# Optimization experiments

Hardware: AMD Instinct MI355X
Metric: run time of the kernel (lower is better)

## Reference

```python
import jax, jax.numpy as jnp
import numpy as np

NEG_INF = -1e12  # matches masked_fill value -1000000000000.0
LEAKY_SLOPE = 0.2


def setup_inputs() -> dict:
    key = jax.random.key(0)
    k1, k2, k3, k4, k5 = jax.random.split(key, 5)
    B, C, H, N, F_IN, F_OUT = 4, 4, 4, 1024, 64, 64
    h = jax.random.normal(k1, (B, C, N, F_IN), dtype=jnp.float32)
    adj = jax.random.randint(k2, (B, N, N), 0, 2).astype(jnp.float32)
    w = jax.random.normal(k3, (C, H, F_IN, F_OUT), dtype=jnp.float32) * 0.1
    a_src = jax.random.normal(k4, (C, H, F_OUT, 1), dtype=jnp.float32) * 0.1
    a_dst = jax.random.normal(k5, (C, H, F_OUT, 1), dtype=jnp.float32) * 0.1
    return {"h": h, "adj": adj, "w": w, "a_src": a_src, "a_dst": a_dst}


def reference(h, adj, w, a_src, a_dst):
    # h: [B,C,N,f_in], w: [C,H,f_in,f_out] -> h_prime: [B,C,H,N,f_out]
    h_prime = jnp.einsum('bcnf,chfo->bchno', h, w)
    t = jnp.tanh(h_prime)
    # additive attention scores: [B,C,H,N]
    attn_src = jnp.einsum('bchno,cho->bchn', t, a_src[..., 0])
    attn_dst = jnp.einsum('bchno,cho->bchn', t, a_dst[..., 0])
    # attn[b,c,h,i,j] = src[i] + dst[j]  -> [B,C,H,N,N]
    attn = attn_src[..., :, None] + attn_dst[..., None, :]
    attn = jnp.where(attn >= 0, attn, LEAKY_SLOPE * attn)  # leaky_relu(0.2)
    N = h.shape[2]
    adj_sl = adj + jnp.eye(N, dtype=adj.dtype)  # add self-loops
    mask = (adj_sl == 0)[:, None, None, :, :]   # [B,1,1,N,N]
    attn = jnp.where(mask, NEG_INF, attn)
    attn = jax.nn.softmax(attn, axis=-1)
    # dropout is identity (attn_dropout=0.0 / eval mode)
    out = jnp.einsum('bchnm,bchmo->bchno', attn, h_prime)
    return out
```

## Files before the change

### kernel.cpp

```cpp
#include <hip/hip_runtime.h>
#include <hip/hip_bf16.h>
#include <math.h>

#define NB 4
#define NC 4
#define NH 4
#define NN 1024
#define NF 64
#define NCOMBO 64
#define LEAK 0.2f

typedef __attribute__((ext_vector_type(8)))  short  short8;
typedef __attribute__((ext_vector_type(16))) float  float16;

static __device__ __forceinline__ unsigned pk_bf16(float a, float b) {
    union { __hip_bfloat162 h; unsigned u; } cv;
    cv.h = __float22bfloat162_rn(make_float2(a, b));
    return cv.u;
}

static __device__ __forceinline__ float fast_tanh(float x) {
    const float e = __expf(2.f * x);
    return 1.f - 2.f * __builtin_amdgcn_rcpf(1.f + e);
}

static __device__ __forceinline__ void async_cp16(const void* gsrc, void* ldst) {
    __builtin_amdgcn_global_load_lds(
        (const __attribute__((address_space(1))) unsigned int*)gsrc,
        (__attribute__((address_space(3))) unsigned int*)ldst, 16, 0, 0);
}

__global__ __launch_bounds__(256) void gA_produce(
    const float* __restrict__ h, const float* __restrict__ adj,
    const float* __restrict__ w, const float* __restrict__ a_src,
    const float* __restrict__ a_dst,
    unsigned short* __restrict__ hpt, float* __restrict__ asrc,
    float* __restrict__ edPt, float* __restrict__ edNt,
    unsigned long long* __restrict__ bits)
{
    __shared__ __align__(16) char smem[33536];
    float* hT     = (float*)smem;
    float* w_s    = (float*)(smem + 16640);
    float* as_lds = (float*)(smem + 33024);
    float* ad_lds = (float*)(smem + 33280);

    const int idx  = blockIdx.x;
    const int t    = threadIdx.x;
    const int g    = (idx & 7)*8 + ((idx >> 3) & 7);
    const int tile = idx >> 6;
    const int b = g >> 4, c = (g >> 2) & 3, hh = g & 3;
    const int tr = t >> 4, tc = t & 15;

    const float4* wsrc = (const float4*)(w + ((size_t)(c*NH + hh))*NF*NF);
    #pragma unroll
    for (int i = 0; i < 4; ++i)
        ((float4*)w_s)[t + i*256] = wsrc[t + i*256];
    if (t < NF) {
        as_lds[t] = a_src[(c*NH + hh)*NF + t];
        ad_lds[t] = a_dst[(c*NH + hh)*NF + t];
    }
    const float* hsrc = h + (((size_t)(b*NC + c))*NN + tile*64)*NF;
    #pragma unroll
    for (int i = 0; i < 4; ++i) {
        const int r = (t >> 4) + i*16, f4 = (t & 15)*4;
        const float4 v = *(const float4*)&hsrc[r*NF + f4];
        hT[(f4+0)*65 + r] = v.x; hT[(f4+1)*65 + r] = v.y;
        hT[(f4+2)*65 + r] = v.z; hT[(f4+3)*65 + r] = v.w;
    }
    __syncthreads();

    float acc[4][4] = {{0.f}};
    #pragma unroll 8
    for (int f = 0; f < 64; ++f) {
        const float4 hv = *(const float4*)&hT[f*65 + tr*4];
        const float4 wv = *(const float4*)&w_s[f*64 + tc*4];
        acc[0][0] = fmaf(hv.x, wv.x, acc[0][0]);
        acc[0][1] = fmaf(hv.x, wv.y, acc[0][1]);
        acc[0][2] = fmaf(hv.x, wv.z, acc[0][2]);
        acc[0][3] = fmaf(hv.x, wv.w, acc[0][3]);
        acc[1][0] = fmaf(hv.y, wv.x, acc[1][0]);
        acc[1][1] = fmaf(hv.y, wv.y, acc[1][1]);
        acc[1][2] = fmaf(hv.y, wv.z, acc[1][2]);
        acc[1][3] = fmaf(hv.y, wv.w, acc[1][3]);
        acc[2][0] = fmaf(hv.z, wv.x, acc[2][0]);
        acc[2][1] = fmaf(hv.z, wv.y, acc[2][1]);
        acc[2][2] = fmaf(hv.z, wv.z, acc[2][2]);
        acc[2][3] = fmaf(hv.z, wv.w, acc[2][3]);
        acc[3][0] = fmaf(hv.w, wv.x, acc[3][0]);
        acc[3][1] = fmaf(hv.w, wv.y, acc[3][1]);
        acc[3][2] = fmaf(hv.w, wv.z, acc[3][2]);
        acc[3][3] = fmaf(hv.w, wv.w, acc[3][3]);
    }

    float ps[4] = {0.f,0.f,0.f,0.f}, pd[4] = {0.f,0.f,0.f,0.f};
    #pragma unroll
    for (int r = 0; r < 4; ++r)
        #pragma unroll
        for (int cc = 0; cc < 4; ++cc) {
            const float tt = fast_tanh(acc[r][cc]);
            ps[r] = fmaf(tt, as_lds[tc*4+cc], ps[r]);
            pd[r] = fmaf(tt, ad_lds[tc*4+cc], pd[r]);
        }
    __syncthreads();
    float* redS = (float*)smem;
    float* redD = redS + 1024;
    #pragma unroll
    for (int r = 0; r < 4; ++r) {
        redS[(tr*4+r)*16 + tc] = ps[r];
        redD[(tr*4+r)*16 + tc] = pd[r];
    }
    __syncthreads();
    if (t < 64) {
        float4 s0 = *(const float4*)&redS[t*16],   s1 = *(const float4*)&redS[t*16+4];
        float4 s2 = *(const float4*)&redS[t*16+8], s3 = *(const float4*)&redS[t*16+12];
        asrc[(size_t)g*NN + tile*64 + t] =
            (s0.x+s0.y+s0.z+s0.w) + (s1.x+s1.y+s1.z+s1.w) +
            (s2.x+s2.y+s2.z+s2.w) + (s3.x+s3.y+s3.z+s3.w);
        float4 d0 = *(const float4*)&redD[t*16],   d1 = *(const float4*)&redD[t*16+4];
        float4 d2 = *(const float4*)&redD[t*16+8], d3 = *(const float4*)&redD[t*16+12];
        const float dsum =
            (d0.x+d0.y+d0.z+d0.w) + (d1.x+d1.y+d1.z+d1.w) +
            (d2.x+d2.y+d2.z+d2.w) + (d3.x+d3.y+d3.z+d3.w);
        edPt[(size_t)g*NN + tile*64 + t] = __expf(dsum);
        edNt[(size_t)g*NN + tile*64 + t] = __expf(LEAK*dsum);
    }
    #pragma unroll
    for (int cc = 0; cc < 4; ++cc) {
        const int o = tc*4 + cc;
        const int pos = (((((tr>>2)*2 + (o>>5))*2 + ((tr>>1)&1))*32 + (o&31))*8)
                        + (tr&1)*4;
        uint2 pk;
        pk.x = pk_bf16(acc[0][cc], acc[1][cc]);
        pk.y = pk_bf16(acc[2][cc], acc[3][cc]);
        *(uint2*)&hpt[((size_t)g*16 + tile)*4096 + pos] = pk;
    }

    {
        const int base = idx*4096;
        #pragma unroll
        for (int q = 0; q < 16; ++q) {
            const int e  = base + q*256 + t;
            const int j  = e & (NN-1);
            const int i  = (e >> 10) & (NN-1);
            const int bb = e >> 20;
            const bool pred = (adj[e] != 0.f) || (j == i);
            const unsigned long long m = __ballot(pred);
            if ((t & 63) == 0) bits[((size_t)bb*NN + i)*16 + (j >> 6)] = m;
        }
    }
}

__global__ __launch_bounds__(256, 4) void gC_attn(
    const unsigned short* __restrict__ hpt, const float* __restrict__ asrc,
    const float* __restrict__ edPt, const float* __restrict__ edNt,
    const unsigned long long* __restrict__ bits, float* __restrict__ out)
{
    __shared__ __align__(16) char smem[29696];
    unsigned short* fragB = (unsigned short*)smem;
    unsigned*       tbl   = (unsigned*)(smem + 16384);
    float*          comb  = (float*)smem;
    unsigned long long* bits_lds = (unsigned long long*)(smem + 20480);
    float*          psum2 = (float*)(smem + 29184);

    const int idx = blockIdx.x;
    const int t   = threadIdx.x;
    const int g   = (idx & 7)*8 + ((idx >> 3) & 7);
    const int it  = idx >> 6;
    const int b   = g >> 4;
    const int i0  = it*64;
    const int wv = t >> 6, lane = t & 63;
    const int l31 = lane & 31, half = lane >> 5;
    const int rg = wv >> 1, jh = wv & 1;
    const int myrow = rg*32 + l31;

    {
        const char* gs = (const char*)hpt + ((size_t)g*16)*8192 + wv*2048 + lane*16;
        char* ls = smem + wv*2048;
        async_cp16(gs, ls);
        async_cp16(gs + 1024, ls + 1024);
    }
    #pragma unroll
    for (int q = 0; q < 4; ++q) {
        const int j = q*256 + t;
        tbl[j] = pk_bf16(edNt[(size_t)g*NN + j], edPt[(size_t)g*NN + j]);
    }
    {
        const unsigned long long* bsrc = bits + ((size_t)b*NN + i0)*16;
        #pragma unroll
        for (int q = 0; q < 4; ++q) {
            const int e = q*256 + t;
            bits_lds[(e >> 4)*17 + (e & 15)] = bsrc[e];
        }
    }
    const float sv    = asrc[(size_t)g*NN + i0 + myrow];
    const float ratio = __expf((LEAK - 1.f)*sv);

    union { short8 v; unsigned short u[8]; } ONES;
    #pragma unroll
    for (int i = 0; i < 8; ++i) ONES.u[i] = 0x3F80;

    float16 acc0, acc1, acc2;
    #pragma unroll
    for (int i = 0; i < 16; ++i) { acc0[i] = 0.f; acc1[i] = 0.f; acc2[i] = 0.f; }

    for (int jt = 0; jt < 16; ++jt) {
        __syncthreads();
        const int fb = jt & 1;
        if (jt < 15) {
            const char* gs = (const char*)hpt + ((size_t)g*16 + jt + 1)*8192
                             + wv*2048 + lane*16;
            char* ls = smem + ((jt + 1) & 1)*8192 + wv*2048;
            async_cp16(gs, ls);
            async_cp16(gs + 1024, ls + 1024);
        }
        const unsigned long long wb = bits_lds[myrow*17 + jt];

        #pragma unroll
        for (int kk = 0; kk < 2; ++kk) {
            const int ks = jh*2 + kk;
            const int jo = ks*16 + half*8;
            const uint4 Ta = *(const uint4*)&tbl[jt*64 + jo];
            const uint4 Tb = *(const uint4*)&tbl[jt*64 + jo + 4];
            const short8 b0 = *(const short8*)
                &fragB[fb*4096 + (((ks*2 + 0)*2 + half)*32 + l31)*8];
            const short8 b1 = *(const short8*)
                &fragB[fb*4096 + (((ks*2 + 1)*2 + half)*32 + l31)*8];
            const unsigned bb = (unsigned)(wb >> jo) & 0xffu;

            float p0, p1, p2, p3, p4, p5, p6, p7;
            {
                union { unsigned u; float f; } hi, lo;
                hi.u = Ta.x & 0xffff0000u; lo.u = Ta.x << 16;
                p0 = fmaxf(hi.f, ratio*lo.f); p0 = (bb & 1u)   ? p0 : 0.f;
                hi.u = Ta.y & 0xffff0000u; lo.u = Ta.y << 16;
                p1 = fmaxf(hi.f, ratio*lo.f); p1 = (bb & 2u)   ? p1 : 0.f;
                hi.u = Ta.z & 0xffff0000u; lo.u = Ta.z << 16;
                p2 = fmaxf(hi.f, ratio*lo.f); p2 = (bb & 4u)   ? p2 : 0.f;
                hi.u = Ta.w & 0xffff0000u; lo.u = Ta.w << 16;
                p3 = fmaxf(hi.f, ratio*lo.f); p3 = (bb & 8u)   ? p3 : 0.f;
                hi.u = Tb.x & 0xffff0000u; lo.u = Tb.x << 16;
                p4 = fmaxf(hi.f, ratio*lo.f); p4 = (bb & 16u)  ? p4 : 0.f;
                hi.u = Tb.y & 0xffff0000u; lo.u = Tb.y << 16;
                p5 = fmaxf(hi.f, ratio*lo.f); p5 = (bb & 32u)  ? p5 : 0.f;
                hi.u = Tb.z & 0xffff0000u; lo.u = Tb.z << 16;
                p6 = fmaxf(hi.f, ratio*lo.f); p6 = (bb & 64u)  ? p6 : 0.f;
                hi.u = Tb.w & 0xffff0000u; lo.u = Tb.w << 16;
                p7 = fmaxf(hi.f, ratio*lo.f); p7 = (bb & 128u) ? p7 : 0.f;
            }

            union { short8 v; unsigned u[4]; } af;
            af.u[0] = pk_bf16(p0, p1);
            af.u[1] = pk_bf16(p2, p3);
            af.u[2] = pk_bf16(p4, p5);
            af.u[3] = pk_bf16(p6, p7);

            acc2 = __builtin_amdgcn_mfma_f32_32x32x16_bf16(af.v, ONES.v, acc2, 0, 0, 0);
            acc0 = __builtin_amdgcn_mfma_f32_32x32x16_bf16(af.v, b0,     acc0, 0, 0, 0);
            acc1 = __builtin_amdgcn_mfma_f32_32x32x16_bf16(af.v, b1,     acc1, 0, 0, 0);
        }
    }

    __syncthreads();

    if (l31 == 0) {
        #pragma unroll
        for (int reg = 0; reg < 16; ++reg) {
            const int r = (reg & 3) + 8*(reg >> 2) + 4*half;
            psum2[jh*64 + rg*32 + r] = acc2[reg];
        }
    }
    if (jh == 1) {
        float* cb = comb + (rg*64 + lane)*34;
        #pragma unroll
        for (int i = 0; i < 8; ++i) {
            float2 v0; v0.x = acc0[2*i]; v0.y = acc0[2*i+1];
            float2 v1; v1.x = acc1[2*i]; v1.y = acc1[2*i+1];
            *(float2*)&cb[2*i]      = v0;
            *(float2*)&cb[16 + 2*i] = v1;
        }
    }
    __syncthreads();
    if (jh == 0) {
        const float* cb = comb + (rg*64 + lane)*34;
        #pragma unroll
        for (int i = 0; i < 8; ++i) {
            const float2 v0 = *(const float2*)&cb[2*i];
            const float2 v1 = *(const float2*)&cb[16 + 2*i];
            acc0[2*i] += v0.x; acc0[2*i+1] += v0.y;
            acc1[2*i] += v1.x; acc1[2*i+1] += v1.y;
        }
        #pragma unroll
        for (int reg = 0; reg < 16; ++reg) {
            const int r = (reg & 3) + 8*(reg >> 2) + 4*half;
            const int row = rg*32 + r;
            const float inv = __builtin_amdgcn_rcpf(psum2[row] + psum2[64 + row]);
            const size_t base = ((size_t)g*NN + i0 + row)*NF;
            out[base + l31]      = acc0[reg] * inv;
            out[base + l31 + 32] = acc1[reg] * inv;
        }
    }
}

extern "C" void kernel_launch(void* const* d_in, const int* in_sizes, int n_in,
                              void* d_out, int out_size, void* d_ws, size_t ws_size,
                              hipStream_t stream)
{
    const float* h     = (const float*)d_in[0];
    const float* adj   = (const float*)d_in[1];
    const float* w     = (const float*)d_in[2];
    const float* a_src = (const float*)d_in[3];
    const float* a_dst = (const float*)d_in[4];
    float* out = (float*)d_out;

    char* ws = (char*)d_ws;
    unsigned short* hpt = (unsigned short*)ws;
    float* asrc         = (float*)(ws + 8388608);
    float* edP          = (float*)(ws + 8388608 + 262144);
    float* edN          = (float*)(ws + 8388608 + 524288);
    unsigned long long* bits = (unsigned long long*)(ws + 8388608 + 786432);

    gA_produce<<<dim3(1024), dim3(256), 0, stream>>>(
        h, adj, w, a_src, a_dst, hpt, asrc, edP, edN, bits);
    gC_attn<<<dim3(1024), dim3(256), 0, stream>>>(
        hpt, asrc, edP, edN, bits, out);
}
```

Measured before the change: 133.5 us.

## Compute h·W projection with split-bf16 MFMA instead of FP32 FMAs

Replaces the scalar FP32 register-tiled GEMM in the producer kernel with 32x32x16 bf16 MFMA instructions, using a hi/lo bf16 split (three MFMAs per k-step) to keep near-FP32 accuracy. The tanh plus attention-vector reductions move to wave shuffles, and the LDS footprint shrinks because h is loaded straight into registers rather than transposed through shared memory. The goal is to cut ALU time in the projection. It adds split/pack overhead and extra syncs, and the producer is probably a small part of the total runtime compared with the attention kernel.

Result: faster. 118.6 us (-11.2%).

```diff
diff --git a/kernel.cpp b/kernel.cpp
--- a/kernel.cpp
+++ b/kernel.cpp
@@ -28,6 +28,25 @@
     __builtin_amdgcn_global_load_lds(
         (const __attribute__((address_space(1))) unsigned int*)gsrc,
         (__attribute__((address_space(3))) unsigned int*)ldst, 16, 0, 0);
+}
+
+static __device__ __forceinline__ void split8(const float4 a, const float4 b,
+                                              short8* hi, short8* lo) {
+    union { short8 v; unsigned u[4]; } H, L;
+    const float x[8] = {a.x,a.y,a.z,a.w,b.x,b.y,b.z,b.w};
+    float lov[8];
+    #pragma unroll
+    for (int p = 0; p < 4; ++p) {
+        const unsigned pk = pk_bf16(x[2*p], x[2*p+1]);
+        H.u[p] = pk;
+        union { unsigned u; float f; } f0, f1;
+        f0.u = pk << 16; f1.u = pk & 0xffff0000u;
+        lov[2*p]   = x[2*p]   - f0.f;
+        lov[2*p+1] = x[2*p+1] - f1.f;
+    }
+    #pragma unroll
+    for (int p = 0; p < 4; ++p) L.u[p] = pk_bf16(lov[2*p], lov[2*p+1]);
+    *hi = H.v; *lo = L.v;
 }
 
 __global__ __launch_bounds__(256) void gA_produce(
@@ -38,18 +57,22 @@
     float* __restrict__ edPt, float* __restrict__ edNt,
     unsigned long long* __restrict__ bits)
 {
-    __shared__ __align__(16) char smem[33536];
-    float* hT     = (float*)smem;
-    float* w_s    = (float*)(smem + 16640);
-    float* as_lds = (float*)(smem + 33024);
-    float* ad_lds = (float*)(smem + 33280);
+    __shared__ __align__(16) char smem[17920];
+    float* w_s    = (float*)smem;
+    unsigned short* whi = (unsigned short*)smem;
+    unsigned short* wlo = (unsigned short*)(smem + 8192);
+    float* as_lds = (float*)(smem + 16384);
+    float* ad_lds = (float*)(smem + 16640);
+    float* scS    = (float*)(smem + 16896);
+    float* scD    = (float*)(smem + 17408);
 
     const int idx  = blockIdx.x;
     const int t    = threadIdx.x;
     const int g    = (idx & 7)*8 + ((idx >> 3) & 7);
     const int tile = idx >> 6;
     const int b = g >> 4, c = (g >> 2) & 3, hh = g & 3;
-    const int tr = t >> 4, tc = t & 15;
+    const int lane = t & 63, l31 = lane & 31, half = lane >> 5;
+    const int wv = t >> 6, rg = wv >> 1, oh = wv & 1;
 
     const float4* wsrc = (const float4*)(w + ((size_t)(c*NH + hh))*NF*NF);
     #pragma unroll
@@ -59,80 +82,109 @@
         as_lds[t] = a_src[(c*NH + hh)*NF + t];
         ad_lds[t] = a_dst[(c*NH + hh)*NF + t];
     }
-    const float* hsrc = h + (((size_t)(b*NC + c))*NN + tile*64)*NF;
-    #pragma unroll
-    for (int i = 0; i < 4; ++i) {
-        const int r = (t >> 4) + i*16, f4 = (t & 15)*4;
-        const float4 v = *(const float4*)&hsrc[r*NF + f4];
-        hT[(f4+0)*65 + r] = v.x; hT[(f4+1)*65 + r] = v.y;
-        hT[(f4+2)*65 + r] = v.z; hT[(f4+3)*65 + r] = v.w;
-    }
-    __syncthreads();
-
-    float acc[4][4] = {{0.f}};
-    #pragma unroll 8
-    for (int f = 0; f < 64; ++f) {
-        const float4 hv = *(const float4*)&hT[f*65 + tr*4];
-        const float4 wv = *(const float4*)&w_s[f*64 + tc*4];
-        acc[0][0] = fmaf(hv.x, wv.x, acc[0][0]);
-        acc[0][1] = fmaf(hv.x, wv.y, acc[0][1]);
-        acc[0][2] = fmaf(hv.x, wv.z, acc[0][2]);
-        acc[0][3] = fmaf(hv.x, wv.w, acc[0][3]);
-        acc[1][0] = fmaf(hv.y, wv.x, acc[1][0]);
-        acc[1][1] = fmaf(hv.y, wv.y, acc[1][1]);
-        acc[1][2] = fmaf(hv.y, wv.z, acc[1][2]);
-        acc[1][3] = fmaf(hv.y, wv.w, acc[1][3]);
-        acc[2][0] = fmaf(hv.z, wv.x, acc[2][0]);
-        acc[2][1] = fmaf(hv.z, wv.y, acc[2][1]);
-        acc[2][2] = fmaf(hv.z, wv.z, acc[2][2]);
-        acc[2][3] = fmaf(hv.z, wv.w, acc[2][3]);
-        acc[3][0] = fmaf(hv.w, wv.x, acc[3][0]);
-        acc[3][1] = fmaf(hv.w, wv.y, acc[3][1]);
-        acc[3][2] = fmaf(hv.w, wv.z, acc[3][2]);
-        acc[3][3] = fmaf(hv.w, wv.w, acc[3][3]);
-    }
-
-    float ps[4] = {0.f,0.f,0.f,0.f}, pd[4] = {0.f,0.f,0.f,0.f};
-    #pragma unroll
-    for (int r = 0; r < 4; ++r)
-        #pragma unroll
-        for (int cc = 0; cc < 4; ++cc) {
-            const float tt = fast_tanh(acc[r][cc]);
-            ps[r] = fmaf(tt, as_lds[tc*4+cc], ps[r]);
-            pd[r] = fmaf(tt, ad_lds[tc*4+cc], pd[r]);
-        }
-    __syncthreads();
-    float* redS = (float*)smem;
-    float* redD = redS + 1024;
-    #pragma unroll
-    for (int r = 0; r < 4; ++r) {
-        redS[(tr*4+r)*16 + tc] = ps[r];
-        redD[(tr*4+r)*16 + tc] = pd[r];
+    __syncthreads();
+
+    float wv0[8], wv1[8];
+    {
+        const int n = t & 31;
+        #pragma unroll
+        for (int j = 0; j < 8; ++j) {
+            const int blk0 = t >> 5, blk1 = (t >> 5) + 8;
+            const int k0 = (blk0 >> 2)*16 + (blk0 & 1)*8 + j;
+            const int o0 = ((blk0 >> 1) & 1)*32 + n;
+            const int k1 = (blk1 >> 2)*16 + (blk1 & 1)*8 + j;
+            const int o1 = ((blk1 >> 1) & 1)*32 + n;
+            wv0[j] = w_s[k0*64 + o0];
+            wv1[j] = w_s[k1*64 + o1];
+        }
+    }
+    short8 ahi[4], alo[4];
+    {
+        const float* hrow = h +
+            (((size_t)(b*NC + c))*NN + tile*64 + rg*32 + l31)*NF;
+        #pragma unroll
+        for (int s = 0; s < 4; ++s) {
+            const float4 v0 = *(const float4*)&hrow[s*16 + half*8];
+            const float4 v1 = *(const float4*)&hrow[s*16 + half*8 + 4];
+            split8(v0, v1, &ahi[s], &alo[s]);
+        }
+    }
+    __syncthreads();
+
+    {
+        union { short8 v; unsigned u[4]; } H; short8 L;
+        float4 a0 = make_float4(wv0[0],wv0[1],wv0[2],wv0[3]);
+        float4 a1 = make_float4(wv0[4],wv0[5],wv0[6],wv0[7]);
+        split8(a0, a1, &H.v, &L);
+        *(short8*)&whi[((t >> 5)*32 + (t & 31))*8] = H.v;
+        *(short8*)&wlo[((t >> 5)*32 + (t & 31))*8] = L;
+        a0 = make_float4(wv1[0],wv1[1],wv1[2],wv1[3]);
+        a1 = make_float4(wv1[4],wv1[5],wv1[6],wv1[7]);
+        split8(a0, a1, &H.v, &L);
+        *(short8*)&whi[(((t >> 5) + 8)*32 + (t & 31))*8] = H.v;
+        *(short8*)&wlo[(((t >> 5) + 8)*32 + (t & 31))*8] = L;
+    }
+    __syncthreads();
+
+    float16 acc;
+    #pragma unroll
+    for (int i = 0; i < 16; ++i) acc[i] = 0.f;
+    #pragma unroll
+    for (int s = 0; s < 4; ++s) {
+        const short8 bhi = *(const short8*)&whi[(((s*2 + oh)*2 + half)*32 + l31)*8];
+        const short8 blo = *(const short8*)&wlo[(((s*2 + oh)*2 + half)*32 + l31)*8];
+        acc = __builtin_amdgcn_mfma_f32_32x32x16_bf16(ahi[s], bhi, acc, 0, 0, 0);
+        acc = __builtin_amdgcn_mfma_f32_32x32x16_bf16(alo[s], bhi, acc, 0, 0, 0);
+        acc = __builtin_amdgcn_mfma_f32_32x32x16_bf16(ahi[s], blo, acc, 0, 0, 0);
+    }
+
+    {
+        const int col = oh*32 + l31;
+        const float av = as_lds[col], dv = ad_lds[col];
+        float sS[16], sD[16];
+        #pragma unroll
+        for (int reg = 0; reg < 16; ++reg) {
+            const float tt = fast_tanh(acc[reg]);
+            sS[reg] = tt * av;
+            sD[reg] = tt * dv;
+        }
+        #pragma unroll
+        for (int off = 1; off <= 16; off <<= 1) {
+            #pragma unroll
+            for (int reg = 0; reg < 16; ++reg) {
+                sS[reg] += __shfl_xor(sS[reg], off);
+                sD[reg] += __shfl_xor(sD[reg], off);
+            }
+        }
+        if (l31 == 0) {
+            #pragma unroll
+            for (int reg = 0; reg < 16; ++reg) {
+                const int row = rg*32 + (reg & 3) + 8*(reg >> 2) + 4*half;
+                scS[row*2 + oh] = sS[reg];
+                scD[row*2 + oh] = sD[reg];
+            }
+        }
+    }
+
+    {
+        unsigned short* dst = hpt + ((size_t)(g*16 + tile))*4096;
+        #pragma unroll
+        for (int q = 0; q < 4; ++q) {
+            const int ks = rg*2 + (q >> 1), hf = q & 1;
+            const int elem = (((ks*2 + oh)*2 + hf)*32 + l31)*8 + 4*half;
+            uint2 pk;
+            pk.x = pk_bf16(acc[q*4 + 0], acc[q*4 + 1]);
+            pk.y = pk_bf16(acc[q*4 + 2], acc[q*4 + 3]);
+            *(uint2*)&dst[elem] = pk;
+        }
     }
     __syncthreads();
     if (t < 64) {
-        float4 s0 = *(const float4*)&redS[t*16],   s1 = *(const float4*)&redS[t*16+4];
-        float4 s2 = *(const float4*)&redS[t*16+8], s3 = *(const float4*)&redS[t*16+12];
-        asrc[(size_t)g*NN + tile*64 + t] =
-            (s0.x+s0.y+s0.z+s0.w) + (s1.x+s1.y+s1.z+s1.w) +
-            (s2.x+s2.y+s2.z+s2.w) + (s3.x+s3.y+s3.z+s3.w);
-        float4 d0 = *(const float4*)&redD[t*16],   d1 = *(const float4*)&redD[t*16+4];
-        float4 d2 = *(const float4*)&redD[t*16+8], d3 = *(const float4*)&redD[t*16+12];
-        const float dsum =
-            (d0.x+d0.y+d0.z+d0.w) + (d1.x+d1.y+d1.z+d1.w) +
-            (d2.x+d2.y+d2.z+d2.w) + (d3.x+d3.y+d3.z+d3.w);
-        edPt[(size_t)g*NN + tile*64 + t] = __expf(dsum);
-        edNt[(size_t)g*NN + tile*64 + t] = __expf(LEAK*dsum);
-    }
-    #pragma unroll
-    for (int cc = 0; cc < 4; ++cc) {
-        const int o = tc*4 + cc;
-        const int pos = (((((tr>>2)*2 + (o>>5))*2 + ((tr>>1)&1))*32 + (o&31))*8)
-                        + (tr&1)*4;
-        uint2 pk;
-        pk.x = pk_bf16(acc[0][cc], acc[1][cc]);
-        pk.y = pk_bf16(acc[2][cc], acc[3][cc]);
-        *(uint2*)&hpt[((size_t)g*16 + tile)*4096 + pos] = pk;
+        const float s = scS[t*2] + scS[t*2 + 1];
+        const float d = scD[t*2] + scD[t*2 + 1];
+        asrc[(size_t)g*NN + tile*64 + t] = s;
+        edPt[(size_t)g*NN + tile*64 + t] = __expf(d);
+        edNt[(size_t)g*NN + tile*64 + t] = __expf(LEAK*d);
     }
 
     {
```
